# Kernel optimization log

Hardware: AMD Instinct MI355X
Metric: run time of the kernel (lower is better)

The kernel has to match this reference:

```python
import jax, jax.numpy as jnp
import numpy as np

TOP_K = 2


def setup_inputs() -> dict:
    key = jax.random.key(0)
    ks = jax.random.split(key, 10)
    B, S, H, E = 4, 2048, 1024, 8
    s = 1.0 / np.sqrt(H)
    x = jax.random.normal(ks[0], (B, S, H), dtype=jnp.float32)
    gate_w = jax.random.normal(ks[1], (H, E), dtype=jnp.float32) * s
    gate_b = jnp.zeros((E,), dtype=jnp.float32)
    w1 = jax.random.normal(ks[2], (E, H, H), dtype=jnp.float32) * s
    b1 = jnp.zeros((E, H), dtype=jnp.float32)
    w2 = jax.random.normal(ks[3], (E, H, H), dtype=jnp.float32) * s
    b2 = jnp.zeros((E, H), dtype=jnp.float32)
    w3 = jax.random.normal(ks[4], (E, H, H), dtype=jnp.float32) * s
    b3 = jnp.zeros((E, H), dtype=jnp.float32)
    return {"x": x, "gate_w": gate_w, "gate_b": gate_b,
            "w1": w1, "b1": b1, "w2": w2, "b2": b2, "w3": w3, "b3": b3}


def reference(x, gate_w, gate_b, w1, b1, w2, b2, w3, b3):
    B, S, H = x.shape
    t = x.reshape(-1, H)                                  # [T, H]
    T = t.shape[0]
    # Router: logits -> fp32 softmax -> top-k -> renormalize
    router_logits = t @ gate_w + gate_b                   # [T, E]
    probs = jax.nn.softmax(router_logits.astype(jnp.float32), axis=-1)
    w, idx = jax.lax.top_k(probs, TOP_K)                  # [T, K]
    w = w / jnp.sum(w, axis=-1, keepdims=True)
    w = w.astype(x.dtype)
    # Dense combine weights: cw[t, e] = router weight if expert e selected for token t, else 0
    rows = jnp.arange(T)[:, None]
    cw = jnp.zeros(router_logits.shape, dtype=x.dtype).at[rows, idx].add(w)  # [T, E]
    # Expert MLPs (relu(fc1) -> relu(fc2) -> fc3), batched over experts
    h1 = jax.nn.relu(jnp.einsum('th,ehf->etf', t, w1) + b1[:, None, :])
    h2 = jax.nn.relu(jnp.einsum('etf,efg->etg', h1, w2) + b2[:, None, :])
    y = jnp.einsum('etg,egh->eth', h2, w3) + b3[:, None, :]                 # [E, T, H]
    # Weighted combine (equivalent to per-expert gather + weighted index_add)
    out = jnp.einsum('te,eth->th', cw, y)                 # [T, H]
    return out.reshape(B, S, H), router_logits
```

## Files before the change

kernel.cpp:

```cpp
#include <hip/hip_runtime.h>
#include <hip/hip_bf16.h>


#define HDIM 1024
#define NEXP 8
#define BM 128
#define BN 128
#define BK 32
#define HH ((size_t)HDIM * HDIM)

typedef __hip_bfloat16 bf16;
typedef unsigned short ushort_t;
typedef __attribute__((ext_vector_type(8))) short bf16x8;
typedef __attribute__((ext_vector_type(4))) float f32x4;

__device__ __forceinline__ float bflo(unsigned u) { return __uint_as_float(u << 16); }
__device__ __forceinline__ float bfhi(unsigned u) { return __uint_as_float(u & 0xffff0000u); }
__device__ __forceinline__ unsigned short f2bfu(float f) {
  bf16 h = __float2bfloat16(f);
  return *reinterpret_cast<unsigned short*>(&h);
}
__device__ __forceinline__ int iclamp(int v, int lo, int hi) {
  return v < lo ? lo : (v > hi ? hi : v);
}

__device__ __forceinline__ void async_cp16(const void* g, void* l) {
  __builtin_amdgcn_global_load_lds((const __attribute__((address_space(1))) void*)g,
                                   (__attribute__((address_space(3))) void*)l,
                                   16, 0, 0);
}

__device__ __forceinline__ void ld4f(const void* base, size_t idx, bool f32, float o[4]) {
  if (f32) {
    float4 v = *(const float4*)((const float*)base + idx);
    o[0] = v.x; o[1] = v.y; o[2] = v.z; o[3] = v.w;
  } else {
    uint2 v = *(const uint2*)((const unsigned short*)base + idx);
    o[0] = bflo(v.x); o[1] = bfhi(v.x); o[2] = bflo(v.y); o[3] = bfhi(v.y);
  }
}

__global__ void k_sniff(const ushort_t* a0, int n0, const ushort_t* a1, int n1,
                        const ushort_t* a2, int n2, const ushort_t* a3, int n3,
                        const ushort_t* a4, int n4, int* __restrict__ meta) {
  int b = blockIdx.x;
  int tid = threadIdx.x;
  if (b >= 5) {
    int idx = (b - 5) * 256 + tid;
    int i = idx < 2048 ? idx : idx + 5;
    if (i < 3072) meta[i] = 0;
    return;
  }
  const ushort_t* a = b == 0 ? a0 : b == 1 ? a1 : b == 2 ? a2 : b == 3 ? a3 : a4;
  int n = b == 0 ? n0 : b == 1 ? n1 : b == 2 ? n2 : b == 3 ? n3 : n4;
  int hits = 0;
  for (int i = tid; i < n; i += 256) {
    ushort_t v = a[i];
    if ((v & 0x7F80) == 0x7F80) hits++;
  }
  __shared__ int red[256];
  red[tid] = hits;
  __syncthreads();
  for (int off = 128; off >= 1; off >>= 1) {
    if (tid < off) red[tid] += red[tid + off];
    __syncthreads();
  }
  if (tid == 0) meta[2048 + b] = red[0];
}

__global__ __launch_bounds__(512) void k_router(
    const void* __restrict__ x, const void* __restrict__ gw,
    const bf16* __restrict__ gb, void* __restrict__ dout, bf16* __restrict__ xb,
    int* __restrict__ sel_e, float* __restrict__ sel_w,
    int* __restrict__ meta, int TS, int T) {
  __shared__ float sgT[NEXP][HDIM];
  const int* flags = meta + 2048;
  bool fx = flags[0] != 0, fgw = flags[1] != 0;
  int tid = threadIdx.x;

#pragma unroll
  for (int r = 0; r < 2; r++) {
    int h = r * 512 + tid;
    float g[8];
    ld4f(gw, (size_t)h * NEXP, fgw, g);
    ld4f(gw, (size_t)h * NEXP + 4, fgw, g + 4);
#pragma unroll
    for (int e = 0; e < NEXP; e++) sgT[e][h] = g[e];
  }
  __syncthreads();

  int wave = tid >> 6, lane = tid & 63;
  int t = blockIdx.x * 8 + wave;

  double acc[NEXP];
#pragma unroll
  for (int e = 0; e < NEXP; e++) acc[e] = 0.0;

  if (t < T) {
#pragma unroll
    for (int j = 0; j < 4; j++) {
      int h = j * 256 + lane * 4;
      float xf[4];
      ld4f(x, (size_t)t * HDIM + h, fx, xf);
      if (fx) {
        uint2 ov;
        ov.x = (unsigned)f2bfu(xf[0]) | ((unsigned)f2bfu(xf[1]) << 16);
        ov.y = (unsigned)f2bfu(xf[2]) | ((unsigned)f2bfu(xf[3]) << 16);
        *(uint2*)((unsigned short*)xb + (size_t)t * HDIM + h) = ov;
      }
#pragma unroll
      for (int e = 0; e < NEXP; e++) {
        float4 g = *(const float4*)&sgT[e][h];
        acc[e] += (double)xf[0] * (double)g.x + (double)xf[1] * (double)g.y
                + (double)xf[2] * (double)g.z + (double)xf[3] * (double)g.w;
      }
    }
  }

#pragma unroll
  for (int off = 32; off >= 1; off >>= 1) {
#pragma unroll
    for (int e = 0; e < NEXP; e++) acc[e] += __shfl_down(acc[e], off);
  }

  if (lane == 0 && t < T) {
    double l[NEXP];
#pragma unroll
    for (int e = 0; e < NEXP; e++) l[e] = acc[e] + (double)__bfloat162float(gb[e]);
    size_t lo = (size_t)T * HDIM + (size_t)t * NEXP;
    if (fx) {
      float* lp = (float*)dout + lo;
#pragma unroll
      for (int e = 0; e < NEXP; e++) lp[e] = (float)l[e];
    } else {
      unsigned short* lp = (unsigned short*)dout + lo;
#pragma unroll
      for (int e = 0; e < NEXP; e++) lp[e] = f2bfu((float)l[e]);
    }
    int i1 = 0; double v1 = l[0];
#pragma unroll
    for (int e = 1; e < NEXP; e++) if (l[e] > v1) { v1 = l[e]; i1 = e; }
    int i2 = -1; double v2 = -1e300;
#pragma unroll
    for (int e = 0; e < NEXP; e++) if (e != i1 && l[e] > v2) { v2 = l[e]; i2 = e; }
    if (i2 < 0) i2 = (i1 + 1) & 7;
    float w1 = 1.0f / (1.0f + __expf((float)(v2 - v1)));
    sel_e[2 * t] = i1; sel_e[2 * t + 1] = i2;
    sel_w[2 * t] = w1; sel_w[2 * t + 1] = 1.0f - w1;
  }
}

__global__ void k_offsets(const int* __restrict__ sel_e, int* __restrict__ meta,
                          int* __restrict__ list, int* __restrict__ row_e,
                          int RCAP, int NTMAX, int TS) {
  int s = blockIdx.x;
  __shared__ int base[NEXP + 1];
  __shared__ int wsum[4][NEXP];
  int tid = threadIdx.x;

  int cnt[NEXP];
#pragma unroll
  for (int e = 0; e < NEXP; e++) cnt[e] = 0;
  const int* se = sel_e + (size_t)2 * s * TS;
  for (int i = tid; i < 2 * TS; i += 256) {
    int v = se[i];
#pragma unroll
    for (int e = 0; e < NEXP; e++) cnt[e] += (v == e) ? 1 : 0;
  }
#pragma unroll
  for (int off = 32; off >= 1; off >>= 1)
#pragma unroll
    for (int e = 0; e < NEXP; e++) cnt[e] += __shfl_down(cnt[e], off);
  int lane = tid & 63, wave = tid >> 6;
  if (lane == 0) {
#pragma unroll
    for (int e = 0; e < NEXP; e++) wsum[wave][e] = cnt[e];
  }
  __syncthreads();

  if (tid == 0) {
    int b = 0;
    for (int e = 0; e < NEXP; e++) {
      int ce = wsum[0][e] + wsum[1][e] + wsum[2][e] + wsum[3][e];
      base[e] = b;
      meta[s * 8 + e] = ce;
      meta[512 + s * 8 + e] = b;
      meta[1024 + s * 8 + e] = b;
      b = (b + ce + BM - 1) & ~(BM - 1);
    }
    base[NEXP] = b;
    meta[2560 + s] = b / BM;
  }
  __syncthreads();

  for (int r = tid; r < NTMAX; r += blockDim.x) {
    int rs = r * BM;
    int e = 0;
    for (int q = 1; q < NEXP; q++) if (rs >= base[q]) e = q;
    row_e[s * NTMAX + r] = e;
  }
  int* ls = list + (size_t)s * RCAP;
  for (int e = 0; e < NEXP; e++) {
    int ce = wsum[0][e] + wsum[1][e] + wsum[2][e] + wsum[3][e];
    for (int p = base[e] + ce + tid; p < base[e + 1]; p += blockDim.x)
      ls[p] = s * TS;
  }
}

__global__ void k_scatter(const int* __restrict__ sel_e, int* __restrict__ meta,
                          int* __restrict__ list, int* __restrict__ pos_of,
                          int T, int TS, int RCAP) {
  __shared__ int lcnt[NEXP];
  __shared__ int lbase[NEXP];
  int tid = threadIdx.x;
  if (tid < NEXP) lcnt[tid] = 0;
  __syncthreads();
  int t = blockIdx.x * blockDim.x + tid;
  int s = (int)(((long long)blockIdx.x * blockDim.x) / TS);
  int e0 = sel_e[2 * t], e1 = sel_e[2 * t + 1];
  int r0 = atomicAdd(&lcnt[e0], 1);
  int r1 = atomicAdd(&lcnt[e1], 1);
  __syncthreads();
  if (tid < NEXP) lbase[tid] = atomicAdd(&meta[512 + s * 8 + tid], lcnt[tid]);
  __syncthreads();
  int p0 = lbase[e0] + r0;
  int p1 = lbase[e1] + r1;
  if (p0 >= 0 && p0 < RCAP) list[(size_t)s * RCAP + p0] = t;
  if (p1 >= 0 && p1 < RCAP) list[(size_t)s * RCAP + p1] = t;
  pos_of[2 * t] = p0;
  pos_of[2 * t + 1] = p1;
}

__global__ void k_trans(const void* __restrict__ wa, const void* __restrict__ wb,
                        const void* __restrict__ wc, const int* __restrict__ flags,
                        bf16* __restrict__ wt) {
  int z = blockIdx.z;
  int layer = z >> 3, e = z & 7;
  const void* w = layer == 0 ? wa : layer == 1 ? wb : wc;
  bool fW = flags[2 + layer] != 0;
  bf16* wtl = wt + (size_t)layer * NEXP * HH;
  __shared__ unsigned short tile[32][33];
  int tid = threadIdx.x;
  int r = tid >> 3, c4 = (tid & 7) * 4;
  int R0 = blockIdx.y * 32, C0 = blockIdx.x * 32;
  float v[4];
  ld4f(w, (size_t)e * HH + (size_t)(R0 + r) * HDIM + C0 + c4, fW, v);
  tile[c4 + 0][r] = f2bfu(v[0]);
  tile[c4 + 1][r] = f2bfu(v[1]);
  tile[c4 + 2][r] = f2bfu(v[2]);
  tile[c4 + 3][r] = f2bfu(v[3]);
  __syncthreads();
  uint2 ov;
  ov.x = (unsigned)tile[r][c4 + 0] | ((unsigned)tile[r][c4 + 1] << 16);
  ov.y = (unsigned)tile[r][c4 + 2] | ((unsigned)tile[r][c4 + 3] << 16);
  *(uint2*)((unsigned short*)wtl + (size_t)e * HH + (size_t)(C0 + r) * HDIM + R0 + c4) = ov;
}

template <bool GATHER, bool RELU>
__global__ __launch_bounds__(256) void k_gemm(
    const bf16* __restrict__ A, const bf16* __restrict__ Axb,
    const int* __restrict__ list,
    const int* __restrict__ row_e, const int* __restrict__ ntiles,
    const bf16* __restrict__ wt, const bf16* __restrict__ bias,
    bf16* __restrict__ C, const int* __restrict__ flags, int Tm1) {
  int id = blockIdx.y * gridDim.x + blockIdx.x;
  int tm = id % gridDim.y;
  int tn = id / gridDim.y;
  if (tm >= *ntiles) return;
  int e = row_e[tm];
  int row0 = tm * BM;
  const bf16* Ause = (GATHER && flags[0] != 0) ? Axb : A;

  const int BUF = (BM + BN) * BK;
  __shared__ __align__(16) unsigned short smem[4 * (BM + BN) * BK];

  int tid = threadIdx.x;
  int lane = tid & 63, wave = tid >> 6;
  int ksw = ((lane & 3) ^ ((lane >> 3) & 3)) * 8;
  int r0 = wave * 32 + (lane >> 2);

  const unsigned short* pb0 = (const unsigned short*)wt + (size_t)e * HH
                            + (size_t)(tn * BN + r0) * HDIM + ksw;
  const unsigned short* pb1 = pb0 + (size_t)16 * HDIM;
  const unsigned short* pa0;
  const unsigned short* pa1;
  if (GATHER) {
    int t0 = iclamp(list[row0 + r0], 0, Tm1);
    int t1 = iclamp(list[row0 + r0 + 16], 0, Tm1);
    pa0 = (const unsigned short*)Ause + (size_t)t0 * HDIM + ksw;
    pa1 = (const unsigned short*)Ause + (size_t)t1 * HDIM + ksw;
  } else {
    pa0 = (const unsigned short*)Ause + (size_t)(row0 + r0) * HDIM + ksw;
    pa1 = pa0 + (size_t)16 * HDIM;
  }
  unsigned short* laD0 = smem + (wave * 32) * BK;
  unsigned short* laD1 = laD0 + 16 * BK;
  unsigned short* lbD0 = smem + BM * BK + (wave * 32) * BK;
  unsigned short* lbD1 = lbD0 + 16 * BK;

#define STAGE(pb, ktt)                                         \
  do {                                                         \
    int _o = (pb) * BUF;                                       \
    async_cp16(pa0 + (size_t)(ktt) * BK, laD0 + _o);           \
    async_cp16(pa1 + (size_t)(ktt) * BK, laD1 + _o);           \
    async_cp16(pb0 + (size_t)(ktt) * BK, lbD0 + _o);           \
    async_cp16(pb1 + (size_t)(ktt) * BK, lbD1 + _o);           \
  } while (0)

  f32x4 acc[4][4];
#pragma unroll
  for (int i = 0; i < 4; i++)
#pragma unroll
    for (int j = 0; j < 4; j++) acc[i][j] = (f32x4){0.f, 0.f, 0.f, 0.f};

  int lm = lane & 15, quad = lane >> 4;
  int am = (wave & 1) * 64, bn = (wave >> 1) * 64;
  int rdc = (quad ^ ((lm >> 1) & 3)) * 8;

  STAGE(0, 0);
  STAGE(1, 1);
  STAGE(2, 2);

  const int NK = HDIM / BK;
  for (int kt = 0; kt < NK; ++kt) {
    int p = kt & 3;
    if (kt < NK - 2)       asm volatile("s_waitcnt vmcnt(8)" ::: "memory");
    else if (kt == NK - 2) asm volatile("s_waitcnt vmcnt(4)" ::: "memory");
    else                   asm volatile("s_waitcnt vmcnt(0)" ::: "memory");
    __builtin_amdgcn_sched_barrier(0);
    __builtin_amdgcn_s_barrier();
    __builtin_amdgcn_sched_barrier(0);
    if (kt + 3 < NK) STAGE((kt + 3) & 3, kt + 3);

    int o = p * BUF;
    bf16x8 af[4], bfr[4];
#pragma unroll
    for (int i = 0; i < 4; i++)
      af[i] = *(const bf16x8*)&smem[o + (am + i * 16 + lm) * BK + rdc];
#pragma unroll
    for (int j = 0; j < 4; j++)
      bfr[j] = *(const bf16x8*)&smem[o + BM * BK + (bn + j * 16 + lm) * BK + rdc];
    __builtin_amdgcn_s_setprio(1);
#pragma unroll
    for (int i = 0; i < 4; i++)
#pragma unroll
      for (int j = 0; j < 4; j++)
        acc[i][j] = __builtin_amdgcn_mfma_f32_16x16x32_bf16(af[i], bfr[j], acc[i][j], 0, 0, 0);
    __builtin_amdgcn_s_setprio(0);
  }
#undef STAGE

  __syncthreads();
  unsigned short* cst = smem;
#pragma unroll
  for (int j = 0; j < 4; j++) {
    int col = bn + j * 16 + lm;
    float bv = __bfloat162float(bias[e * HDIM + tn * BN + col]);
#pragma unroll
    for (int i = 0; i < 4; i++) {
      int rowb = am + i * 16 + quad * 4;
#pragma unroll
      for (int rr = 0; rr < 4; rr++) {
        float v = acc[i][j][rr] + bv;
        if (RELU) v = fmaxf(v, 0.f);
        cst[(rowb + rr) * BN + col] = f2bfu(v);
      }
    }
  }
  __syncthreads();
  {
    unsigned short* Cg = (unsigned short*)C;
#pragma unroll
    for (int it = 0; it < 8; it++) {
      int o = it * 4096 + tid * 16;
      int row = o >> 8;
      int cole = (o & 255) >> 1;
      uint4 v = *(const uint4*)((const char*)cst + o);
      *(uint4*)&Cg[(size_t)(row0 + row) * HDIM + tn * BN + cole] = v;
    }
  }
}

__global__ void k_combine(const bf16* __restrict__ y, const int* __restrict__ pos_of,
                          const float* __restrict__ sel_w, void* __restrict__ dout,
                          size_t out_elem_off, const int* __restrict__ meta, int Pm1) {
  bool fx = meta[2048] != 0;
  int t = blockIdx.x;
  int tid = threadIdx.x;
  int p0 = iclamp(pos_of[2 * t], 0, Pm1);
  int p1 = iclamp(pos_of[2 * t + 1], 0, Pm1);
  float w0 = sel_w[2 * t], w1 = sel_w[2 * t + 1];
  int h = tid * 4;
  uint2 a = *(const uint2*)((const unsigned short*)y + (size_t)p0 * HDIM + h);
  uint2 b = *(const uint2*)((const unsigned short*)y + (size_t)p1 * HDIM + h);
  float o0 = w0 * bflo(a.x) + w1 * bflo(b.x);
  float o1 = w0 * bfhi(a.x) + w1 * bfhi(b.x);
  float o2 = w0 * bflo(a.y) + w1 * bflo(b.y);
  float o3 = w0 * bfhi(a.y) + w1 * bfhi(b.y);
  size_t off = out_elem_off + (size_t)t * HDIM + h;
  if (fx) {
    float4 ov = { o0, o1, o2, o3 };
    *(float4*)((float*)dout + off) = ov;
  } else {
    uint2 ov;
    ov.x = (unsigned)f2bfu(o0) | ((unsigned)f2bfu(o1) << 16);
    ov.y = (unsigned)f2bfu(o2) | ((unsigned)f2bfu(o3) << 16);
    *(uint2*)((unsigned short*)dout + off) = ov;
  }
}

extern "C" void kernel_launch(void* const* d_in, const int* in_sizes, int n_in,
                              void* d_out, int out_size, void* d_ws, size_t ws_size,
                              hipStream_t stream) {
  const void* x  = d_in[0];
  const void* gw = d_in[1];
  const bf16* gb = (const bf16*)d_in[2];
  const void* w1 = d_in[3];
  const bf16* b1 = (const bf16*)d_in[4];
  const void* w2 = d_in[5];
  const bf16* b2 = (const bf16*)d_in[6];
  const void* w3 = d_in[7];
  const bf16* b3 = (const bf16*)d_in[8];

  const int T = in_sizes[0] / HDIM;
  const size_t wtsz = (size_t)NEXP * HH * 2;
  const size_t xbsz = (size_t)T * HDIM * 2;

  int S = 64;
  size_t base_need = 0;
  for (int cand = 1; cand <= 64; cand *= 2) {
    size_t rcap = (size_t)2 * T / cand + NEXP * BM;
    size_t ntmx = rcap / BM;
    size_t need = 12288 + (size_t)8 * T * 3 + (size_t)4 * cand * rcap
                + (size_t)4 * cand * ntmx + wtsz + 2 * rcap * HDIM * 2
                + xbsz + 1024;
    if (need <= ws_size) { S = cand; base_need = need; break; }
  }
  const int TS = T / S;
  const int RCAP = 2 * TS + NEXP * BM;
  const int NTMAX = RCAP / BM;
  const bool merged = (base_need + 2 * wtsz <= ws_size);

  char* ws = (char*)d_ws;
  size_t ofs = 0;
  int*   meta   = (int*)(ws + ofs);   ofs += 12288;
  int*   sel_e  = (int*)(ws + ofs);   ofs += (size_t)8 * T;
  float* sel_w  = (float*)(ws + ofs); ofs += (size_t)8 * T;
  int*   pos_of = (int*)(ws + ofs);   ofs += (size_t)8 * T;
  int*   list   = (int*)(ws + ofs);   ofs += (size_t)4 * S * RCAP;
  int*   row_e  = (int*)(ws + ofs);   ofs += (size_t)4 * S * NTMAX;
  ofs = (ofs + 255) & ~(size_t)255;
  bf16* wt0 = (bf16*)(ws + ofs); ofs += merged ? 3 * wtsz : wtsz;
  bf16* h1  = (bf16*)(ws + ofs); ofs += (size_t)RCAP * HDIM * 2;
  bf16* h2  = (bf16*)(ws + ofs); ofs += (size_t)RCAP * HDIM * 2;
  bf16* xb  = (bf16*)(ws + ofs); ofs += xbsz;
  bf16* wt1 = merged ? wt0 + NEXP * HH : wt0;
  bf16* wt2 = merged ? wt0 + 2 * NEXP * HH : wt0;

  int* flags = meta + 2048;

  k_sniff<<<17, 256, 0, stream>>>((const ushort_t*)x, 32768,
                                  (const ushort_t*)gw, HDIM * NEXP,
                                  (const ushort_t*)w1, 32768,
                                  (const ushort_t*)w2, 32768,
                                  (const ushort_t*)w3, 32768, meta);
  k_router<<<(T + 7) / 8, 512, 0, stream>>>(x, gw, gb, d_out, xb, sel_e, sel_w,
                                            meta, TS, T);
  k_offsets<<<S, 256, 0, stream>>>(sel_e, meta, list, row_e, RCAP, NTMAX, TS);
  {
    int sbd = TS < 256 ? TS : 256;
    k_scatter<<<T / sbd, sbd, 0, stream>>>(sel_e, meta, list, pos_of, T, TS, RCAP);
  }

  dim3 gg(HDIM / BN, NTMAX);
  const bf16* xbf = (const bf16*)x;

  if (merged) {
    dim3 tgm(HDIM / 32, HDIM / 32, 3 * NEXP);
    k_trans<<<tgm, 256, 0, stream>>>(w1, w2, w3, flags, wt0);
  }
  for (int s = 0; s < S; s++) {
    const int* lst = list + (size_t)s * RCAP;
    const int* re  = row_e + (size_t)s * NTMAX;
    const int* nt  = meta + 2560 + s;
    dim3 tg1(HDIM / 32, HDIM / 32, NEXP);
    if (!merged) k_trans<<<tg1, 256, 0, stream>>>(w1, w1, w1, flags + 0, wt0);
    k_gemm<true,  true ><<<gg, 256, 0, stream>>>(xbf, xb, lst, re, nt, wt0, b1, h1, flags, T - 1);
    if (!merged) k_trans<<<tg1, 256, 0, stream>>>(w2, w2, w2, flags + 1, wt1);
    k_gemm<false, true ><<<gg, 256, 0, stream>>>(h1, nullptr, nullptr, re, nt, wt1, b2, h2, flags, T - 1);
    if (!merged) k_trans<<<tg1, 256, 0, stream>>>(w3, w3, w3, flags + 2, wt2);
    k_gemm<false, false><<<gg, 256, 0, stream>>>(h2, nullptr, nullptr, re, nt, wt2, b3, h1, flags, T - 1);
    k_combine<<<TS, 256, 0, stream>>>(h1, pos_of + (size_t)2 * s * TS,
                                      sel_w + (size_t)2 * s * TS,
                                      d_out, (size_t)s * TS * HDIM, meta, RCAP - 1);
  }
}
```

Before: 423.5 us.

## Enlarge expert GEMM tiles to 256x256 with 8 waves and triple buffering

Doubles the GEMM macro-tile to 256x256 and runs it with 512 threads (8 waves arranged 2x4), each wave computing a 128x64 sub-tile. The shared-memory pipeline drops from four to three stages so the larger tiles still fit, and the epilogue writes out the result in two 128-row halves that reuse the staging buffer. The aim is more reuse per loaded byte and higher MFMA density per block. In exchange, padding waste grows in the per-expert row tiles, there are fewer blocks to fill the GPU, and register pressure and pipeline depth both change.

```diff
diff --git a/kernel.cpp b/kernel.cpp
--- a/kernel.cpp
+++ b/kernel.cpp
@@ -4,8 +4,8 @@
 
 #define HDIM 1024
 #define NEXP 8
-#define BM 128
-#define BN 128
+#define BM 256
+#define BN 256
 #define BK 32
 #define HH ((size_t)HDIM * HDIM)
 
@@ -257,7 +257,7 @@
 }
 
 template <bool GATHER, bool RELU>
-__global__ __launch_bounds__(256) void k_gemm(
+__global__ __launch_bounds__(512, 2) void k_gemm(
     const bf16* __restrict__ A, const bf16* __restrict__ Axb,
     const int* __restrict__ list,
     const int* __restrict__ row_e, const int* __restrict__ ntiles,
@@ -272,31 +272,31 @@
   const bf16* Ause = (GATHER && flags[0] != 0) ? Axb : A;
 
   const int BUF = (BM + BN) * BK;
-  __shared__ __align__(16) unsigned short smem[4 * (BM + BN) * BK];
+  __shared__ __align__(16) unsigned short smem[3 * (BM + BN) * BK];
 
   int tid = threadIdx.x;
   int lane = tid & 63, wave = tid >> 6;
   int ksw = ((lane & 3) ^ ((lane >> 3) & 3)) * 8;
-  int r0 = wave * 32 + (lane >> 2);
+  int r0 = wave * 16 + (lane >> 2);
 
   const unsigned short* pb0 = (const unsigned short*)wt + (size_t)e * HH
                             + (size_t)(tn * BN + r0) * HDIM + ksw;
-  const unsigned short* pb1 = pb0 + (size_t)16 * HDIM;
+  const unsigned short* pb1 = pb0 + (size_t)128 * HDIM;
   const unsigned short* pa0;
   const unsigned short* pa1;
   if (GATHER) {
     int t0 = iclamp(list[row0 + r0], 0, Tm1);
-    int t1 = iclamp(list[row0 + r0 + 16], 0, Tm1);
+    int t1 = iclamp(list[row0 + r0 + 128], 0, Tm1);
     pa0 = (const unsigned short*)Ause + (size_t)t0 * HDIM + ksw;
     pa1 = (const unsigned short*)Ause + (size_t)t1 * HDIM + ksw;
   } else {
     pa0 = (const unsigned short*)Ause + (size_t)(row0 + r0) * HDIM + ksw;
-    pa1 = pa0 + (size_t)16 * HDIM;
-  }
-  unsigned short* laD0 = smem + (wave * 32) * BK;
-  unsigned short* laD1 = laD0 + 16 * BK;
-  unsigned short* lbD0 = smem + BM * BK + (wave * 32) * BK;
-  unsigned short* lbD1 = lbD0 + 16 * BK;
+    pa1 = pa0 + (size_t)128 * HDIM;
+  }
+  unsigned short* laD0 = smem + (wave * 16) * BK;
+  unsigned short* laD1 = laD0 + 128 * BK;
+  unsigned short* lbD0 = smem + BM * BK + (wave * 16) * BK;
+  unsigned short* lbD1 = lbD0 + 128 * BK;
 
 #define STAGE(pb, ktt)                                         \
   do {                                                         \
@@ -307,76 +307,77 @@
     async_cp16(pb1 + (size_t)(ktt) * BK, lbD1 + _o);           \
   } while (0)
 
-  f32x4 acc[4][4];
-#pragma unroll
-  for (int i = 0; i < 4; i++)
+  f32x4 acc[8][4];
+#pragma unroll
+  for (int i = 0; i < 8; i++)
 #pragma unroll
     for (int j = 0; j < 4; j++) acc[i][j] = (f32x4){0.f, 0.f, 0.f, 0.f};
 
   int lm = lane & 15, quad = lane >> 4;
-  int am = (wave & 1) * 64, bn = (wave >> 1) * 64;
+  int wr = wave >> 2, wc = wave & 3;
+  int am = wr * 128, bn = wc * 64;
   int rdc = (quad ^ ((lm >> 1) & 3)) * 8;
 
   STAGE(0, 0);
   STAGE(1, 1);
-  STAGE(2, 2);
 
   const int NK = HDIM / BK;
   for (int kt = 0; kt < NK; ++kt) {
-    int p = kt & 3;
-    if (kt < NK - 2)       asm volatile("s_waitcnt vmcnt(8)" ::: "memory");
-    else if (kt == NK - 2) asm volatile("s_waitcnt vmcnt(4)" ::: "memory");
-    else                   asm volatile("s_waitcnt vmcnt(0)" ::: "memory");
+    int p = kt % 3;
+    if (kt < NK - 1) asm volatile("s_waitcnt vmcnt(4)" ::: "memory");
+    else             asm volatile("s_waitcnt vmcnt(0)" ::: "memory");
     __builtin_amdgcn_sched_barrier(0);
     __builtin_amdgcn_s_barrier();
     __builtin_amdgcn_sched_barrier(0);
-    if (kt + 3 < NK) STAGE((kt + 3) & 3, kt + 3);
+    if (kt + 2 < NK) STAGE((kt + 2) % 3, kt + 2);
 
     int o = p * BUF;
-    bf16x8 af[4], bfr[4];
-#pragma unroll
-    for (int i = 0; i < 4; i++)
-      af[i] = *(const bf16x8*)&smem[o + (am + i * 16 + lm) * BK + rdc];
+    bf16x8 bfr[4];
 #pragma unroll
     for (int j = 0; j < 4; j++)
       bfr[j] = *(const bf16x8*)&smem[o + BM * BK + (bn + j * 16 + lm) * BK + rdc];
     __builtin_amdgcn_s_setprio(1);
 #pragma unroll
-    for (int i = 0; i < 4; i++)
+    for (int i = 0; i < 8; i++) {
+      bf16x8 afi = *(const bf16x8*)&smem[o + (am + i * 16 + lm) * BK + rdc];
 #pragma unroll
       for (int j = 0; j < 4; j++)
-        acc[i][j] = __builtin_amdgcn_mfma_f32_16x16x32_bf16(af[i], bfr[j], acc[i][j], 0, 0, 0);
+        acc[i][j] = __builtin_amdgcn_mfma_f32_16x16x32_bf16(afi, bfr[j], acc[i][j], 0, 0, 0);
+    }
     __builtin_amdgcn_s_setprio(0);
   }
 #undef STAGE
 
-  __syncthreads();
   unsigned short* cst = smem;
-#pragma unroll
-  for (int j = 0; j < 4; j++) {
-    int col = bn + j * 16 + lm;
-    float bv = __bfloat162float(bias[e * HDIM + tn * BN + col]);
-#pragma unroll
-    for (int i = 0; i < 4; i++) {
-      int rowb = am + i * 16 + quad * 4;
-#pragma unroll
-      for (int rr = 0; rr < 4; rr++) {
-        float v = acc[i][j][rr] + bv;
-        if (RELU) v = fmaxf(v, 0.f);
-        cst[(rowb + rr) * BN + col] = f2bfu(v);
+  unsigned short* Cg = (unsigned short*)C;
+#pragma unroll
+  for (int hh = 0; hh < 2; hh++) {
+    __syncthreads();
+    if (wr == hh) {
+#pragma unroll
+      for (int j = 0; j < 4; j++) {
+        int col = bn + j * 16 + lm;
+        float bv = __bfloat162float(bias[e * HDIM + tn * BN + col]);
+#pragma unroll
+        for (int i = 0; i < 8; i++) {
+          int rowl = i * 16 + quad * 4;
+#pragma unroll
+          for (int rr = 0; rr < 4; rr++) {
+            float v = acc[i][j][rr] + bv;
+            if (RELU) v = fmaxf(v, 0.f);
+            cst[(rowl + rr) * BN + col] = f2bfu(v);
+          }
+        }
       }
     }
-  }
-  __syncthreads();
-  {
-    unsigned short* Cg = (unsigned short*)C;
+    __syncthreads();
 #pragma unroll
     for (int it = 0; it < 8; it++) {
-      int o = it * 4096 + tid * 16;
-      int row = o >> 8;
-      int cole = (o & 255) >> 1;
+      int o = it * 8192 + tid * 16;
+      int row = o >> 9;
+      int cole = (o & 511) >> 1;
       uint4 v = *(const uint4*)((const char*)cst + o);
-      *(uint4*)&Cg[(size_t)(row0 + row) * HDIM + tn * BN + cole] = v;
+      *(uint4*)&Cg[(size_t)(row0 + hh * 128 + row) * HDIM + tn * BN + cole] = v;
     }
   }
 }
@@ -485,11 +486,11 @@
     const int* nt  = meta + 2560 + s;
     dim3 tg1(HDIM / 32, HDIM / 32, NEXP);
     if (!merged) k_trans<<<tg1, 256, 0, stream>>>(w1, w1, w1, flags + 0, wt0);
-    k_gemm<true,  true ><<<gg, 256, 0, stream>>>(xbf, xb, lst, re, nt, wt0, b1, h1, flags, T - 1);
+    k_gemm<true,  true ><<<gg, 512, 0, stream>>>(xbf, xb, lst, re, nt, wt0, b1, h1, flags, T - 1);
     if (!merged) k_trans<<<tg1, 256, 0, stream>>>(w2, w2, w2, flags + 1, wt1);
-    k_gemm<false, true ><<<gg, 256, 0, stream>>>(h1, nullptr, nullptr, re, nt, wt1, b2, h2, flags, T - 1);
+    k_gemm<false, true ><<<gg, 512, 0, stream>>>(h1, nullptr, nullptr, re, nt, wt1, b2, h2, flags, T - 1);
     if (!merged) k_trans<<<tg1, 256, 0, stream>>>(w3, w3, w3, flags + 2, wt2);
-    k_gemm<false, false><<<gg, 256, 0, stream>>>(h2, nullptr, nullptr, re, nt, wt2, b3, h1, flags, T - 1);
+    k_gemm<false, false><<<gg, 512, 0, stream>>>(h2, nullptr, nullptr, re, nt, wt2, b3, h1, flags, T - 1);
     k_combine<<<TS, 256, 0, stream>>>(h1, pos_of + (size_t)2 * s * TS,
                                       sel_w + (size_t)2 * s * TS,
                                       d_out, (size_t)s * TS * HDIM, meta, RCAP - 1);
```

Result: slower. 446.8 us (+5.5%).
